# Optimization experiments

Hardware: AMD Instinct MI355X
Metric: run time of the kernel (lower is better)

## Reference

```python
import jax, jax.numpy as jnp
import numpy as np

B, V, L, C, H = 2, 8, 256, 1024, 16

def setup_inputs() -> dict:
    key = jax.random.key(0)
    ks = jax.random.split(key, 6)
    s = 0.02  # init scale for weights
    x = jax.random.normal(ks[0], (B, V, L, C), jnp.float32)
    Wq = jax.random.normal(ks[1], (C, C), jnp.float32) * s
    Wk = jax.random.normal(ks[2], (C, C), jnp.float32) * s
    Wv = jax.random.normal(ks[3], (C, C), jnp.float32) * s
    Wp = jax.random.normal(ks[4], (C, C), jnp.float32) * s
    bp = jnp.zeros((C,), jnp.float32)
    return {"x": x, "Wq": Wq, "Wk": Wk, "Wv": Wv, "Wp": Wp, "bp": bp}

def _view_mask(V, L):
    # view-level allow mask, expanded to token level [S, S]
    vi = jnp.arange(V)
    qv, kv = vi[:, None], vi[None, :]
    cross = ((qv == 0) & (kv == 1)) | ((qv == 1) & (kv == 0))
    later = (qv > 1) | (kv > 1)
    allow = cross | (later & (qv >= kv))  # [V, V]
    return jnp.repeat(jnp.repeat(allow, L, axis=0), L, axis=1)  # [V*L, V*L]

def reference(x, Wq, Wk, Wv, Wp, bp):
    b, v, l, c = x.shape
    h = H
    dh = c // h
    scale = dh ** -0.5
    s = v * l
    xf = x.reshape(b, s, c)
    # torch Linear: y = x @ W.T
    q = (xf @ Wq.T).reshape(b, s, h, dh).transpose(0, 2, 1, 3)  # [b,h,s,dh]
    k = (xf @ Wk.T).reshape(b, s, h, dh).transpose(0, 2, 1, 3)
    vv = (xf @ Wv.T).reshape(b, s, h, dh).transpose(0, 2, 1, 3)
    scores = jnp.einsum('bhqd,bhkd->bhqk', q, k) * scale  # [b,h,s,s]
    mask = _view_mask(v, l)
    scores = jnp.where(mask, scores, -jnp.inf)
    attn = jax.nn.softmax(scores, axis=-1)
    out = jnp.einsum('bhqk,bhkd->bhqd', attn, vv)
    out = out.transpose(0, 2, 1, 3).reshape(b, v, l, c)
    return out @ Wp.T + bp
```

## Files before the change

kernel.cpp:

```cpp
#include <hip/hip_runtime.h>
#include <stdint.h>

typedef unsigned short ushort_t;
typedef __attribute__((ext_vector_type(8))) __bf16 bf16x8;
typedef __attribute__((ext_vector_type(4))) float floatx4;

__device__ __forceinline__ ushort_t f2bf(float f) {
    uint32_t u = __builtin_bit_cast(uint32_t, f);
    u += 0x7fffu + ((u >> 16) & 1u);
    return (ushort_t)(u >> 16);
}

typedef __attribute__((address_space(1))) const void glb_void;
typedef __attribute__((address_space(3))) void lds_void;
__device__ __forceinline__ void gld16(const void* g, void* l) {
    __builtin_amdgcn_global_load_lds((glb_void*)g, (lds_void*)l, 16, 0, 0);
}

#define QSCALE 0.18033688011112042f

__global__ void cast_kernel(const float* __restrict__ x,
                            const float* __restrict__ Wq, const float* __restrict__ Wk,
                            const float* __restrict__ Wv, const float* __restrict__ Wp,
                            ushort_t* __restrict__ xb, ushort_t* __restrict__ Wqkvb,
                            ushort_t* __restrict__ Wpb)
{
    const int64_t NX = 4194304, NW = 1048576;
    int64_t i4 = ((int64_t)blockIdx.x * blockDim.x + threadIdx.x) * 4;
    const float* src; ushort_t* dst; int64_t off;
    if (i4 < NX)            { src = x;  dst = xb;          off = i4; }
    else if (i4 < NX+NW)    { src = Wq; dst = Wqkvb;       off = i4 - NX; }
    else if (i4 < NX+2*NW)  { src = Wk; dst = Wqkvb + NW;  off = i4 - NX - NW; }
    else if (i4 < NX+3*NW)  { src = Wv; dst = Wqkvb + 2*NW;off = i4 - NX - 2*NW; }
    else                    { src = Wp; dst = Wpb;         off = i4 - NX - 3*NW; }
    float4 v = *(const float4*)(src + off);
    ushort4 o;
    o.x = f2bf(v.x); o.y = f2bf(v.y); o.z = f2bf(v.z); o.w = f2bf(v.w);
    *(ushort4*)(dst + off) = o;
}

#define BM 128
#define BN 128
#define BK 32

__global__ __launch_bounds__(256, 3)
void gemm_bt(const ushort_t* __restrict__ A, const ushort_t* __restrict__ Bmat,
             int M, int N, int K, int mode,
             ushort_t* __restrict__ qb, ushort_t* __restrict__ kb, ushort_t* __restrict__ vtb,
             float* __restrict__ outf, const float* __restrict__ bias)
{
    __shared__ ushort_t As[BM * BK];
    __shared__ ushort_t Bs[BN * BK];
    const int tid  = threadIdx.x;
    const int lane = tid & 63;
    const int wave = tid >> 6;
    const int m0 = blockIdx.x * BM;
    const int n0 = blockIdx.y * BN;
    const int wrow = (wave >> 1) * 64;
    const int wcol = (wave & 1) * 64;
    const int q_ = lane >> 4;
    const int ml = lane & 15;

    floatx4 acc[4][4];
    for (int i = 0; i < 4; i++) for (int j = 0; j < 4; j++) acc[i][j] = floatx4{0.f,0.f,0.f,0.f};

    const int t0 = wave * 2, t1 = wave * 2 + 1;
    const int row_l = lane >> 2;
    const int col_l = (lane & 3) * 8;
    const ushort_t* Ag0 = A    + (int64_t)(m0 + t0*16 + row_l) * K + col_l;
    const ushort_t* Ag1 = A    + (int64_t)(m0 + t1*16 + row_l) * K + col_l;
    const ushort_t* Bg0 = Bmat + (int64_t)(n0 + t0*16 + row_l) * K + col_l;
    const ushort_t* Bg1 = Bmat + (int64_t)(n0 + t1*16 + row_l) * K + col_l;
    ushort_t* Al0 = As + t0*512; ushort_t* Al1 = As + t1*512;
    ushort_t* Bl0 = Bs + t0*512; ushort_t* Bl1 = Bs + t1*512;

    for (int k0 = 0; k0 < K; k0 += BK) {
        __syncthreads();
        gld16(Ag0 + k0, Al0);
        gld16(Ag1 + k0, Al1);
        gld16(Bg0 + k0, Bl0);
        gld16(Bg1 + k0, Bl1);
        __syncthreads();
        bf16x8 af[4], bf[4];
        for (int mt = 0; mt < 4; mt++)
            af[mt] = *(const bf16x8*)(As + (wrow + mt*16 + ml) * BK + q_*8);
        for (int nt = 0; nt < 4; nt++)
            bf[nt] = *(const bf16x8*)(Bs + (wcol + nt*16 + ml) * BK + q_*8);
        for (int mt = 0; mt < 4; mt++)
            for (int nt = 0; nt < 4; nt++)
                acc[mt][nt] = __builtin_amdgcn_mfma_f32_16x16x32_bf16(af[mt], bf[nt], acc[mt][nt], 0, 0, 0);
    }

    if (mode == 0) {
        for (int mt = 0; mt < 4; mt++) for (int nt = 0; nt < 4; nt++) {
            floatx4 v = acc[mt][nt];
            int col = n0 + wcol + nt*16 + ml;
            int which = col >> 10;
            int nn = col & 1023;
            int h = nn >> 6, d = nn & 63;
            if (which < 2) {
                ushort_t* dst = (which == 0) ? qb : kb;
                float sc = (which == 0) ? QSCALE : 1.0f;
                for (int r = 0; r < 4; r++) {
                    int rowg = m0 + wrow + mt*16 + q_*4 + r;
                    int b = rowg >> 11, s = rowg & 2047;
                    dst[(((int64_t)(b*16 + h) * 2048 + s) << 6) + d] = f2bf(v[r] * sc);
                }
            } else {
                int rowg0 = m0 + wrow + mt*16 + q_*4;
                int b = rowg0 >> 11, sbase = rowg0 & 2047;
                ushort4 o;
                o.x = f2bf(v[0]); o.y = f2bf(v[1]); o.z = f2bf(v[2]); o.w = f2bf(v[3]);
                *(ushort4*)(vtb + (((int64_t)(b*16 + h) * 64 + d) << 11) + sbase) = o;
            }
        }
    } else {
        for (int mt = 0; mt < 4; mt++) for (int nt = 0; nt < 4; nt++) {
            floatx4 v = acc[mt][nt];
            int col = n0 + wcol + nt*16 + ml;
            float bv = bias[col];
            for (int r = 0; r < 4; r++) {
                int rowg = m0 + wrow + mt*16 + q_*4 + r;
                outf[(int64_t)rowg * N + col] = v[r] + bv;
            }
        }
    }
}

__global__ __launch_bounds__(256, 3)
void attn_kernel(const ushort_t* __restrict__ Q, const ushort_t* __restrict__ Kb,
                 const ushort_t* __restrict__ Vt, ushort_t* __restrict__ Out)
{
    __shared__ ushort_t Kl[8192];
    __shared__ ushort_t Vl[8192];
    __shared__ ushort_t Pl[4 * 16 * 136];

    int bi = blockIdx.x;
    int xcd = bi & 7;
    int sl  = bi >> 3;
    int bh  = xcd + 8 * (sl & 3);
    int rest = sl >> 2;
    int qv = 7 - (rest >> 2);
    int qt = rest & 3;
    int b = bh >> 4, h = bh & 15;
    int tid = threadIdx.x;
    int wave = tid >> 6, lane = tid & 63;
    int q_ = lane >> 4, ml = lane & 15;
    int rlane = lane & 15, clane = lane >> 4;
    int s0 = qv*256 + qt*64 + wave*16;

    const ushort_t* Kbh = Kb + ((int64_t)bh << 17);
    const ushort_t* Vbh = Vt + ((int64_t)bh << 17);
    ushort_t* Pw = Pl + wave * (16 * 136);

    const ushort_t* Qp = Q + (((int64_t)bh*2048 + s0 + ml) << 6) + q_*8;
    bf16x8 aq0 = *(const bf16x8*)(Qp);
    bf16x8 aq1 = *(const bf16x8*)(Qp + 32);

    floatx4 o_acc[4];
    for (int i = 0; i < 4; i++) o_acc[i] = floatx4{0.f,0.f,0.f,0.f};
    float lsum[4] = {0.f, 0.f, 0.f, 0.f};

    int views[8]; int nviews;
    if      (qv == 0) { views[0] = 1; nviews = 1; }
    else if (qv == 1) { views[0] = 0; nviews = 1; }
    else { nviews = qv + 1; for (int i = 0; i < nviews; i++) views[i] = i; }

    for (int vi = 0; vi < nviews; vi++) {
        int kb0 = views[vi] * 256;
        for (int ck = 0; ck < 2; ck++) {
            int koff = kb0 + ck * 128;

            __syncthreads();
            for (int i = 0; i < 4; i++) {
                int id = wave*4 + i;
                const ushort_t* gk = Kbh + (((int64_t)(koff + (id >> 1)*16 + rlane)) << 6)
                                         + (id & 1)*32 + clane*8;
                gld16(gk, Kl + id*512);
                const ushort_t* gv = Vbh + ((int64_t)((id & 3)*16 + rlane) << 11)
                                         + koff + (id >> 2)*32 + clane*8;
                gld16(gv, Vl + id*512);
            }
            __syncthreads();

            floatx4 sc[8];
            for (int kt = 0; kt < 8; kt++) {
                bf16x8 k0 = *(const bf16x8*)(Kl + kt*1024 + lane*8);
                bf16x8 k1 = *(const bf16x8*)(Kl + kt*1024 + 512 + lane*8);
                floatx4 cz = floatx4{0.f,0.f,0.f,0.f};
                cz = __builtin_amdgcn_mfma_f32_16x16x32_bf16(aq0, k0, cz, 0, 0, 0);
                cz = __builtin_amdgcn_mfma_f32_16x16x32_bf16(aq1, k1, cz, 0, 0, 0);
                sc[kt] = cz;
            }

            for (int kt = 0; kt < 8; kt++)
                for (int r = 0; r < 4; r++) {
                    float p = __builtin_amdgcn_exp2f(sc[kt][r]);
                    lsum[r] += p;
                    Pw[(q_*4 + r)*136 + kt*16 + ml] = f2bf(p);
                }

            asm volatile("s_waitcnt lgkmcnt(0)" ::: "memory");

            for (int g = 0; g < 4; g++) {
                bf16x8 ap = *(const bf16x8*)(Pw + ml*136 + g*32 + q_*8);
                for (int dt = 0; dt < 4; dt++) {
                    bf16x8 vv = *(const bf16x8*)(Vl + (g*4 + dt)*512 + lane*8);
                    o_acc[dt] = __builtin_amdgcn_mfma_f32_16x16x32_bf16(ap, vv, o_acc[dt], 0, 0, 0);
                }
            }
        }
    }

    for (int off = 1; off < 16; off <<= 1)
        for (int r = 0; r < 4; r++)
            lsum[r] += __shfl_xor(lsum[r], off);

    for (int dt = 0; dt < 4; dt++)
        for (int r = 0; r < 4; r++) {
            float v = o_acc[dt][r] / lsum[r];
            int sr = s0 + q_*4 + r;
            Out[((int64_t)b*2048 + sr) * 1024 + h*64 + dt*16 + ml] = f2bf(v);
        }
}

extern "C" void kernel_launch(void* const* d_in, const int* in_sizes, int n_in,
                              void* d_out, int out_size, void* d_ws, size_t ws_size,
                              hipStream_t stream) {
    const float* x  = (const float*)d_in[0];
    const float* Wq = (const float*)d_in[1];
    const float* Wk = (const float*)d_in[2];
    const float* Wv = (const float*)d_in[3];
    const float* Wp = (const float*)d_in[4];
    const float* bp = (const float*)d_in[5];
    float* out = (float*)d_out;

    char* ws = (char*)d_ws;
    ushort_t* xb    = (ushort_t*)(ws);
    ushort_t* Wqkvb = (ushort_t*)(ws + ((size_t)8  << 20));
    ushort_t* Wpb   = (ushort_t*)(ws + ((size_t)14 << 20));
    ushort_t* qb    = (ushort_t*)(ws + ((size_t)16 << 20));
    ushort_t* kbuf  = (ushort_t*)(ws + ((size_t)24 << 20));
    ushort_t* vtb   = (ushort_t*)(ws + ((size_t)40 << 20));
    ushort_t* attno = xb;

    cast_kernel<<<8192, 256, 0, stream>>>(x, Wq, Wk, Wv, Wp, xb, Wqkvb, Wpb);

    dim3 g0(4096 / BM, 3072 / BN);
    gemm_bt<<<g0, 256, 0, stream>>>(xb, Wqkvb, 4096, 3072, 1024, 0,
                                    qb, kbuf, vtb, nullptr, nullptr);

    attn_kernel<<<1024, 256, 0, stream>>>(qb, kbuf, vtb, attno);

    dim3 g1(4096 / BM, 1024 / BN);
    gemm_bt<<<g1, 256, 0, stream>>>(attno, Wpb, 4096, 1024, 1024, 1,
                                    nullptr, nullptr, nullptr, out, bp);
}
```

Before: 185.1 us.

## Load V fragments directly from global, transpose QK MFMA, fuse exp with packed P stores

The attention kernel stops staging V in LDS and reads each wave's V operand fragments straight from global memory, which frees LDS and raises the occupancy target from 3 to 4 blocks per CU. The QK^T MFMA operands are swapped so each lane holds a row's scores, which lets exp, the row-sum and packed 8-byte P stores happen inline per tile and makes the final normalization a few shuffles. s_setprio hints are placed around the MFMA groups. The cost is uncached global V reads inside the PV loop, with latency and repeated traffic across the four waves that LDS used to hide.

```diff
diff --git a/kernel.cpp b/kernel.cpp
--- a/kernel.cpp
+++ b/kernel.cpp
@@ -4,6 +4,7 @@
 typedef unsigned short ushort_t;
 typedef __attribute__((ext_vector_type(8))) __bf16 bf16x8;
 typedef __attribute__((ext_vector_type(4))) float floatx4;
+typedef __attribute__((ext_vector_type(2))) uint32_t uint32x2;
 
 __device__ __forceinline__ ushort_t f2bf(float f) {
     uint32_t u = __builtin_bit_cast(uint32_t, f);
@@ -127,12 +128,11 @@
     }
 }
 
-__global__ __launch_bounds__(256, 3)
+__global__ __launch_bounds__(256, 4)
 void attn_kernel(const ushort_t* __restrict__ Q, const ushort_t* __restrict__ Kb,
                  const ushort_t* __restrict__ Vt, ushort_t* __restrict__ Out)
 {
     __shared__ ushort_t Kl[8192];
-    __shared__ ushort_t Vl[8192];
     __shared__ ushort_t Pl[4 * 16 * 136];
 
     int bi = blockIdx.x;
@@ -157,9 +157,11 @@
     bf16x8 aq0 = *(const bf16x8*)(Qp);
     bf16x8 aq1 = *(const bf16x8*)(Qp + 32);
 
+    const ushort_t* Vr = Vbh + (int64_t)ml*2048 + q_*8;
+
     floatx4 o_acc[4];
     for (int i = 0; i < 4; i++) o_acc[i] = floatx4{0.f,0.f,0.f,0.f};
-    float lsum[4] = {0.f, 0.f, 0.f, 0.f};
+    float lsum = 0.f;
 
     int views[8]; int nviews;
     if      (qv == 0) { views[0] = 1; nviews = 1; }
@@ -172,53 +174,65 @@
             int koff = kb0 + ck * 128;
 
             __syncthreads();
+            #pragma unroll
             for (int i = 0; i < 4; i++) {
                 int id = wave*4 + i;
                 const ushort_t* gk = Kbh + (((int64_t)(koff + (id >> 1)*16 + rlane)) << 6)
                                          + (id & 1)*32 + clane*8;
                 gld16(gk, Kl + id*512);
-                const ushort_t* gv = Vbh + ((int64_t)((id & 3)*16 + rlane) << 11)
-                                         + koff + (id >> 2)*32 + clane*8;
-                gld16(gv, Vl + id*512);
             }
             __syncthreads();
 
-            floatx4 sc[8];
+            #pragma unroll
             for (int kt = 0; kt < 8; kt++) {
                 bf16x8 k0 = *(const bf16x8*)(Kl + kt*1024 + lane*8);
                 bf16x8 k1 = *(const bf16x8*)(Kl + kt*1024 + 512 + lane*8);
                 floatx4 cz = floatx4{0.f,0.f,0.f,0.f};
-                cz = __builtin_amdgcn_mfma_f32_16x16x32_bf16(aq0, k0, cz, 0, 0, 0);
-                cz = __builtin_amdgcn_mfma_f32_16x16x32_bf16(aq1, k1, cz, 0, 0, 0);
-                sc[kt] = cz;
-            }
-
-            for (int kt = 0; kt < 8; kt++)
-                for (int r = 0; r < 4; r++) {
-                    float p = __builtin_amdgcn_exp2f(sc[kt][r]);
-                    lsum[r] += p;
-                    Pw[(q_*4 + r)*136 + kt*16 + ml] = f2bf(p);
-                }
+                __builtin_amdgcn_s_setprio(1);
+                cz = __builtin_amdgcn_mfma_f32_16x16x32_bf16(k0, aq0, cz, 0, 0, 0);
+                cz = __builtin_amdgcn_mfma_f32_16x16x32_bf16(k1, aq1, cz, 0, 0, 0);
+                __builtin_amdgcn_s_setprio(0);
+
+                float p0 = __builtin_amdgcn_exp2f(cz[0]);
+                float p1 = __builtin_amdgcn_exp2f(cz[1]);
+                float p2 = __builtin_amdgcn_exp2f(cz[2]);
+                float p3 = __builtin_amdgcn_exp2f(cz[3]);
+                lsum += (p0 + p1) + (p2 + p3);
+                uint32_t w0 = (uint32_t)f2bf(p0) | ((uint32_t)f2bf(p1) << 16);
+                uint32_t w1 = (uint32_t)f2bf(p2) | ((uint32_t)f2bf(p3) << 16);
+                uint32x2 wv; wv[0] = w0; wv[1] = w1;
+                *(uint32x2*)(Pw + ml*136 + kt*16 + q_*4) = wv;
+            }
 
             asm volatile("s_waitcnt lgkmcnt(0)" ::: "memory");
 
+            const ushort_t* Vc = Vr + koff;
+            #pragma unroll
             for (int g = 0; g < 4; g++) {
                 bf16x8 ap = *(const bf16x8*)(Pw + ml*136 + g*32 + q_*8);
+                __builtin_amdgcn_s_setprio(1);
+                #pragma unroll
                 for (int dt = 0; dt < 4; dt++) {
-                    bf16x8 vv = *(const bf16x8*)(Vl + (g*4 + dt)*512 + lane*8);
+                    bf16x8 vv = *(const bf16x8*)(Vc + dt*32768 + g*32);
                     o_acc[dt] = __builtin_amdgcn_mfma_f32_16x16x32_bf16(ap, vv, o_acc[dt], 0, 0, 0);
                 }
+                __builtin_amdgcn_s_setprio(0);
             }
         }
     }
 
-    for (int off = 1; off < 16; off <<= 1)
-        for (int r = 0; r < 4; r++)
-            lsum[r] += __shfl_xor(lsum[r], off);
-
+    lsum += __shfl_xor(lsum, 16);
+    lsum += __shfl_xor(lsum, 32);
+    float rinv[4];
+    #pragma unroll
+    for (int r = 0; r < 4; r++)
+        rinv[r] = 1.0f / __shfl(lsum, q_*4 + r);
+
+    #pragma unroll
     for (int dt = 0; dt < 4; dt++)
+        #pragma unroll
         for (int r = 0; r < 4; r++) {
-            float v = o_acc[dt][r] / lsum[r];
+            float v = o_acc[dt][r] * rinv[r];
             int sr = s0 + q_*4 + r;
             Out[((int64_t)b*2048 + sr) * 1024 + h*64 + dt*16 + ml] = f2bf(v);
         }
```

New measurement: 230.6 us. 24.6% more time.

## Process 32 query rows per wave in attention to reuse K/V tiles

Applied to the files above, without the earlier changes.

Each attention wave now handles two 16-row query tiles instead of one, so every K/V tile loaded into LDS is reused across 128 query rows per block and the grid halves to 512 blocks. The QK MFMA operands are swapped so that each lane holds scores for a single query row, which lets probabilities be packed and written to LDS as 64-bit stores and reduces the row-sum reduction to two shuffles. The change also adds s_setprio around the MFMA groups, unrolls the loops and reorders the block-to-view mapping to interleave heavy and light views. In exchange it uses more registers and LDS, lowers the occupancy target from 3 to 2, and leaves fewer blocks for load balancing.

```diff
diff --git a/kernel.cpp b/kernel.cpp
--- a/kernel.cpp
+++ b/kernel.cpp
@@ -4,6 +4,7 @@
 typedef unsigned short ushort_t;
 typedef __attribute__((ext_vector_type(8))) __bf16 bf16x8;
 typedef __attribute__((ext_vector_type(4))) float floatx4;
+typedef __attribute__((ext_vector_type(2))) uint32_t uint32x2;
 
 __device__ __forceinline__ ushort_t f2bf(float f) {
     uint32_t u = __builtin_bit_cast(uint32_t, f);
@@ -127,39 +128,40 @@
     }
 }
 
-__global__ __launch_bounds__(256, 3)
+__global__ __launch_bounds__(256, 2)
 void attn_kernel(const ushort_t* __restrict__ Q, const ushort_t* __restrict__ Kb,
                  const ushort_t* __restrict__ Vt, ushort_t* __restrict__ Out)
 {
     __shared__ ushort_t Kl[8192];
     __shared__ ushort_t Vl[8192];
-    __shared__ ushort_t Pl[4 * 16 * 136];
+    __shared__ ushort_t Pl[4 * 32 * 136];
 
     int bi = blockIdx.x;
-    int xcd = bi & 7;
-    int sl  = bi >> 3;
-    int bh  = xcd + 8 * (sl & 3);
-    int rest = sl >> 2;
-    int qv = 7 - (rest >> 2);
-    int qt = rest & 3;
+    int bh = (bi & 7) + 8 * ((bi >> 3) & 3);
+    int qt = (bi >> 5) & 1;
+    int g8 = bi >> 6;
+    int qv = (g8 < 4) ? (7 - g8) : (g8 - 4);
     int b = bh >> 4, h = bh & 15;
     int tid = threadIdx.x;
     int wave = tid >> 6, lane = tid & 63;
     int q_ = lane >> 4, ml = lane & 15;
     int rlane = lane & 15, clane = lane >> 4;
-    int s0 = qv*256 + qt*64 + wave*16;
+    int s0 = qv*256 + qt*128 + wave*32;
 
     const ushort_t* Kbh = Kb + ((int64_t)bh << 17);
     const ushort_t* Vbh = Vt + ((int64_t)bh << 17);
-    ushort_t* Pw = Pl + wave * (16 * 136);
+    ushort_t* Pw = Pl + wave * (32 * 136);
 
     const ushort_t* Qp = Q + (((int64_t)bh*2048 + s0 + ml) << 6) + q_*8;
-    bf16x8 aq0 = *(const bf16x8*)(Qp);
-    bf16x8 aq1 = *(const bf16x8*)(Qp + 32);
-
-    floatx4 o_acc[4];
-    for (int i = 0; i < 4; i++) o_acc[i] = floatx4{0.f,0.f,0.f,0.f};
-    float lsum[4] = {0.f, 0.f, 0.f, 0.f};
+    bf16x8 aq0A = *(const bf16x8*)(Qp);
+    bf16x8 aq1A = *(const bf16x8*)(Qp + 32);
+    bf16x8 aq0B = *(const bf16x8*)(Qp + 1024);
+    bf16x8 aq1B = *(const bf16x8*)(Qp + 1024 + 32);
+
+    floatx4 o_accA[4], o_accB[4];
+    for (int i = 0; i < 4; i++) { o_accA[i] = floatx4{0.f,0.f,0.f,0.f};
+                                  o_accB[i] = floatx4{0.f,0.f,0.f,0.f}; }
+    float lsumA = 0.f, lsumB = 0.f;
 
     int views[8]; int nviews;
     if      (qv == 0) { views[0] = 1; nviews = 1; }
@@ -172,6 +174,7 @@
             int koff = kb0 + ck * 128;
 
             __syncthreads();
+            #pragma unroll
             for (int i = 0; i < 4; i++) {
                 int id = wave*4 + i;
                 const ushort_t* gk = Kbh + (((int64_t)(koff + (id >> 1)*16 + rlane)) << 6)
@@ -183,44 +186,77 @@
             }
             __syncthreads();
 
-            floatx4 sc[8];
+            #pragma unroll
             for (int kt = 0; kt < 8; kt++) {
                 bf16x8 k0 = *(const bf16x8*)(Kl + kt*1024 + lane*8);
                 bf16x8 k1 = *(const bf16x8*)(Kl + kt*1024 + 512 + lane*8);
-                floatx4 cz = floatx4{0.f,0.f,0.f,0.f};
-                cz = __builtin_amdgcn_mfma_f32_16x16x32_bf16(aq0, k0, cz, 0, 0, 0);
-                cz = __builtin_amdgcn_mfma_f32_16x16x32_bf16(aq1, k1, cz, 0, 0, 0);
-                sc[kt] = cz;
-            }
-
-            for (int kt = 0; kt < 8; kt++)
-                for (int r = 0; r < 4; r++) {
-                    float p = __builtin_amdgcn_exp2f(sc[kt][r]);
-                    lsum[r] += p;
-                    Pw[(q_*4 + r)*136 + kt*16 + ml] = f2bf(p);
-                }
+                floatx4 czA = floatx4{0.f,0.f,0.f,0.f};
+                floatx4 czB = floatx4{0.f,0.f,0.f,0.f};
+                __builtin_amdgcn_s_setprio(1);
+                czA = __builtin_amdgcn_mfma_f32_16x16x32_bf16(k0, aq0A, czA, 0, 0, 0);
+                czA = __builtin_amdgcn_mfma_f32_16x16x32_bf16(k1, aq1A, czA, 0, 0, 0);
+                czB = __builtin_amdgcn_mfma_f32_16x16x32_bf16(k0, aq0B, czB, 0, 0, 0);
+                czB = __builtin_amdgcn_mfma_f32_16x16x32_bf16(k1, aq1B, czB, 0, 0, 0);
+                __builtin_amdgcn_s_setprio(0);
+
+                float a0 = __builtin_amdgcn_exp2f(czA[0]);
+                float a1 = __builtin_amdgcn_exp2f(czA[1]);
+                float a2 = __builtin_amdgcn_exp2f(czA[2]);
+                float a3 = __builtin_amdgcn_exp2f(czA[3]);
+                lsumA += (a0 + a1) + (a2 + a3);
+                uint32x2 wa;
+                wa[0] = (uint32_t)f2bf(a0) | ((uint32_t)f2bf(a1) << 16);
+                wa[1] = (uint32_t)f2bf(a2) | ((uint32_t)f2bf(a3) << 16);
+                *(uint32x2*)(Pw + ml*136 + kt*16 + q_*4) = wa;
+
+                float b0 = __builtin_amdgcn_exp2f(czB[0]);
+                float b1 = __builtin_amdgcn_exp2f(czB[1]);
+                float b2 = __builtin_amdgcn_exp2f(czB[2]);
+                float b3 = __builtin_amdgcn_exp2f(czB[3]);
+                lsumB += (b0 + b1) + (b2 + b3);
+                uint32x2 wb;
+                wb[0] = (uint32_t)f2bf(b0) | ((uint32_t)f2bf(b1) << 16);
+                wb[1] = (uint32_t)f2bf(b2) | ((uint32_t)f2bf(b3) << 16);
+                *(uint32x2*)(Pw + (16 + ml)*136 + kt*16 + q_*4) = wb;
+            }
 
             asm volatile("s_waitcnt lgkmcnt(0)" ::: "memory");
 
+            #pragma unroll
             for (int g = 0; g < 4; g++) {
-                bf16x8 ap = *(const bf16x8*)(Pw + ml*136 + g*32 + q_*8);
+                bf16x8 apA = *(const bf16x8*)(Pw + ml*136 + g*32 + q_*8);
+                bf16x8 apB = *(const bf16x8*)(Pw + (16 + ml)*136 + g*32 + q_*8);
+                __builtin_amdgcn_s_setprio(1);
+                #pragma unroll
                 for (int dt = 0; dt < 4; dt++) {
                     bf16x8 vv = *(const bf16x8*)(Vl + (g*4 + dt)*512 + lane*8);
-                    o_acc[dt] = __builtin_amdgcn_mfma_f32_16x16x32_bf16(ap, vv, o_acc[dt], 0, 0, 0);
+                    o_accA[dt] = __builtin_amdgcn_mfma_f32_16x16x32_bf16(apA, vv, o_accA[dt], 0, 0, 0);
+                    o_accB[dt] = __builtin_amdgcn_mfma_f32_16x16x32_bf16(apB, vv, o_accB[dt], 0, 0, 0);
                 }
-            }
-        }
-    }
-
-    for (int off = 1; off < 16; off <<= 1)
-        for (int r = 0; r < 4; r++)
-            lsum[r] += __shfl_xor(lsum[r], off);
-
+                __builtin_amdgcn_s_setprio(0);
+            }
+        }
+    }
+
+    lsumA += __shfl_xor(lsumA, 16);
+    lsumA += __shfl_xor(lsumA, 32);
+    lsumB += __shfl_xor(lsumB, 16);
+    lsumB += __shfl_xor(lsumB, 32);
+    float rinvA[4], rinvB[4];
+    #pragma unroll
+    for (int r = 0; r < 4; r++) {
+        rinvA[r] = 1.0f / __shfl(lsumA, q_*4 + r);
+        rinvB[r] = 1.0f / __shfl(lsumB, q_*4 + r);
+    }
+
+    #pragma unroll
     for (int dt = 0; dt < 4; dt++)
+        #pragma unroll
         for (int r = 0; r < 4; r++) {
-            float v = o_acc[dt][r] / lsum[r];
-            int sr = s0 + q_*4 + r;
-            Out[((int64_t)b*2048 + sr) * 1024 + h*64 + dt*16 + ml] = f2bf(v);
+            int srA = s0 + q_*4 + r;
+            Out[((int64_t)b*2048 + srA) * 1024 + h*64 + dt*16 + ml] = f2bf(o_accA[dt][r] * rinvA[r]);
+            int srB = s0 + 16 + q_*4 + r;
+            Out[((int64_t)b*2048 + srB) * 1024 + h*64 + dt*16 + ml] = f2bf(o_accB[dt][r] * rinvB[r]);
         }
 }
 
@@ -250,7 +286,7 @@
     gemm_bt<<<g0, 256, 0, stream>>>(xb, Wqkvb, 4096, 3072, 1024, 0,
                                     qb, kbuf, vtb, nullptr, nullptr);
 
-    attn_kernel<<<1024, 256, 0, stream>>>(qb, kbuf, vtb, attno);
+    attn_kernel<<<512, 256, 0, stream>>>(qb, kbuf, vtb, attno);
 
     dim3 g1(4096 / BM, 1024 / BN);
     gemm_bt<<<g1, 256, 0, stream>>>(attno, Wpb, 4096, 1024, 1024, 1,
```

Result: slower. 189.8 us (+2.6%).
